# Performance work log

Measured on AMD Instinct MI355X. Metric: run time of the kernel, lower is better.

## Reference

```python
import jax, jax.numpy as jnp
import numpy as np
from jax import lax

N_FFT = 1024
HOP = 256
FFT_BIN = N_FFT // 2 + 1  # 513


def make_stft_kernel(n_fft: int) -> jnp.ndarray:
    """Fixed DFT basis kernel, shape (2*fft_bin, 1, n_fft), windowed with periodic Hann."""
    fft_bin = n_fft // 2 + 1
    # torch.linspace(0, 1, n_fft) is endpoint-inclusive, same as jnp.linspace
    t = jnp.linspace(0.0, 1.0, n_fft, dtype=jnp.float32)[None, None, :]
    k = jnp.arange(fft_bin, dtype=jnp.float32)[:, None, None]
    xt = t * k * (2.0 * jnp.pi)
    kernel = jnp.concatenate([jnp.cos(xt), jnp.sin(xt)], axis=0)  # (2*fft_bin, 1, n_fft)
    # torch.hann_window is periodic: 0.5*(1 - cos(2*pi*n/N))
    n = jnp.arange(n_fft, dtype=jnp.float32)
    hann = 0.5 * (1.0 - jnp.cos(2.0 * jnp.pi * n / n_fft))
    return kernel * hann[None, None, :]


def setup_inputs() -> dict:
    key = jax.random.key(0)
    x = jax.random.normal(key, (16, 1, 262144), dtype=jnp.float32)
    kernel = make_stft_kernel(N_FFT)
    return {"x": x, "kernel": kernel}


def reference(x, kernel):
    # padding == 'center'
    left = N_FFT // 2
    right = N_FFT - left
    x = jnp.pad(x, ((0, 0), (0, 0), (left, right)))
    # strided conv1d with fixed DFT-basis kernel
    y = lax.conv_general_dilated(
        x, kernel,
        window_strides=(HOP,),
        padding='VALID',
        dimension_numbers=('NCW', 'OIW', 'NCW'),
    )  # (B, 2*fft_bin, num_frames)
    real, imag = jnp.split(y, 2, axis=1)
    return real, imag
```

## Files before the change

kernel.cpp:

```cpp
#include <hip/hip_runtime.h>
#include <hip/hip_bf16.h>

#define NFFT    1024
#define HOPSZ   256
#define XLEN    262144
#define PADLEN  (XLEN + NFFT)
#define NBATCH  16
#define NBINS2  1026
#define FBIN    513
#define NFRAMES 1025
#define NGF     (NBATCH * NFRAMES)
#define TOTOUT  ((size_t)NBATCH * FBIN * NFRAMES)

#define KT 64
#define NKT 16
#define NWG 1024
#define BUFE 16384
#define BUFB 32768
#define LDS_BYTES (2 * BUFB)
#define NTAIL  49184
#define PSTRIDE 132

#define PX_BLKS 2056
#define PW_BLKS 1026

typedef short bf16x8 __attribute__((ext_vector_type(8)));
typedef float f32x4  __attribute__((ext_vector_type(4)));
typedef unsigned short u16x8 __attribute__((ext_vector_type(8)));
typedef unsigned short u16x4 __attribute__((ext_vector_type(4)));

__device__ __forceinline__ unsigned short f2bf(float f) {
  union { float f; unsigned u; } v; v.f = f;
  unsigned r = v.u + 0x7fffu + ((v.u >> 16) & 1u);
  return (unsigned short)(r >> 16);
}
__device__ __forceinline__ float bf2f(unsigned short h) {
  union { unsigned u; float f; } v; v.u = ((unsigned)h) << 16; return v.f;
}

typedef __attribute__((address_space(1))) void void_g;
typedef __attribute__((address_space(3))) void void_l;
__device__ __forceinline__ void gload_lds16(const void* g, void* l) {
  __builtin_amdgcn_global_load_lds((void_g*)(g), (void_l*)(l), 16, 0, 0);
}

__global__ __launch_bounds__(256) void pack_kernel(const float* __restrict__ x,
                                                   const float* __restrict__ W,
                                                   unsigned short* __restrict__ xp,
                                                   unsigned short* __restrict__ wb) {
  const int bid = blockIdx.x;
  const int tid = threadIdx.x;
  if (bid < PX_BLKS) {
    long long base = ((long long)bid * 256 + tid) * 8;
    int b   = (int)(base / PADLEN);
    int pos = (int)(base % PADLEN);
    const float* xb = x + (long long)b * XLEN;
    u16x8 v;
#pragma unroll
    for (int j = 0; j < 8; ++j) {
      int xi = pos + j - (NFFT / 2);
      float f = ((unsigned)xi < (unsigned)XLEN) ? xb[xi] : 0.0f;
      v[j] = f2bf(f);
    }
    *reinterpret_cast<u16x8*>(xp + base) = v;
  } else {
    long long t = (((long long)(bid - PX_BLKS)) * 256 + tid) * 4;
    float4 f = *reinterpret_cast<const float4*>(W + t);
    u16x4 v;
    v[0] = f2bf(f.x); v[1] = f2bf(f.y); v[2] = f2bf(f.z); v[3] = f2bf(f.w);
    *reinterpret_cast<u16x4*>(wb + t) = v;
  }
}

__global__ __launch_bounds__(256, 2) void stft_mfma128_kernel(const unsigned short* __restrict__ Xp,
                                                              const unsigned short* __restrict__ Wb,
                                                              float* __restrict__ out) {
  extern __shared__ unsigned short lds[];
  const int tid = threadIdx.x;
  const int l   = tid & 63;
  const int w   = tid >> 6;
  const int wr  = w >> 1;
  const int wc  = w & 1;
  const int r16 = l & 15, hi = l >> 4;

  const int bid   = blockIdx.x;
  const int xcd   = bid & 7;
  const int local = bid >> 3;
  const int nt    = xcd * 16 + (local >> 3);
  const int mt    = local & 7;
  const int bin0  = mt * 128;
  const int gf0   = nt * 128;

  const int lr = l >> 3;
  const int ls = l & 7;
  const int cswz = ((ls ^ lr) << 3);

  unsigned aqoff[4], boff[4];
#pragma unroll
  for (int q = 0; q < 4; ++q)
    aqoff[q] = (unsigned)(bin0 + (w * 4 + q) * 8 + lr) * NFFT + cswz;
#pragma unroll
  for (int j = 0; j < 4; ++j) {
    const int gf = gf0 + (w * 4 + j) * 8 + lr;
    const int bb = gf / NFRAMES;
    const int fr = gf - bb * NFRAMES;
    boff[j] = (unsigned)bb * PADLEN + (unsigned)fr * HOPSZ + cswz;
  }

#define STAGE(D, KC) do { \
    _Pragma("unroll") \
    for (int q_ = 0; q_ < 4; ++q_) \
      gload_lds16(Wb + aqoff[q_] + (KC), lds + (D) * BUFE + (w * 4 + q_) * 512); \
    _Pragma("unroll") \
    for (int j_ = 0; j_ < 4; ++j_) \
      gload_lds16(Xp + boff[j_] + (KC), lds + (D) * BUFE + 8192 + (w * 4 + j_) * 512); \
    } while (0)

  const int aB0 = (wr * 64 + r16) * 128;
  const int bB0 = 16384 + (wc * 64 + r16) * 128;
  const int swz = (r16 & 7) << 4;
  const int c0  = (hi * 16) ^ swz;
  const int c1  = (64 + hi * 16) ^ swz;

#define RD8(BASE, C, AARR, BARR) do { \
    _Pragma("unroll") \
    for (int n_ = 0; n_ < 4; ++n_) \
      BARR[n_] = *reinterpret_cast<const bf16x8*>((const char*)(BASE) + bB0 + n_ * 2048 + (C)); \
    _Pragma("unroll") \
    for (int m_ = 0; m_ < 4; ++m_) \
      AARR[m_] = *reinterpret_cast<const bf16x8*>((const char*)(BASE) + aB0 + m_ * 2048 + (C)); \
    } while (0)

#define MFMA16(AARR, BARR) do { \
    __builtin_amdgcn_s_setprio(1); \
    _Pragma("unroll") \
    for (int m_ = 0; m_ < 4; ++m_) { \
      _Pragma("unroll") \
      for (int n_ = 0; n_ < 4; ++n_) \
        acc[m_][n_] = __builtin_amdgcn_mfma_f32_16x16x32_bf16(AARR[m_], BARR[n_], acc[m_][n_], 0, 0, 0); \
    } \
    __builtin_amdgcn_s_setprio(0); } while (0)

  f32x4 acc[4][4] = {};
  bf16x8 A0[4], B0[4], A1[4], B1[4];

  STAGE(0, 0);
  STAGE(1, KT);
  asm volatile("s_waitcnt vmcnt(8)" ::: "memory");
  __builtin_amdgcn_s_barrier();
  __builtin_amdgcn_sched_barrier(0);
  RD8(lds, c0, A0, B0);

#pragma unroll 1
  for (int t = 0; t < NKT; ++t) {
    const int ci = t & 1;
    const char* cbuf = (const char*)lds + ci * BUFB;
    const char* nbuf = (const char*)lds + (ci ^ 1) * BUFB;
    const int kc2 = (t + 2) << 6;

    RD8(cbuf, c1, A1, B1);
    __builtin_amdgcn_sched_barrier(0);
    asm volatile("s_waitcnt lgkmcnt(8)" ::: "memory");
    __builtin_amdgcn_sched_barrier(0);
    MFMA16(A0, B0);

    asm volatile("s_waitcnt vmcnt(0) lgkmcnt(0)" ::: "memory");
    __builtin_amdgcn_sched_barrier(0);
    __builtin_amdgcn_s_barrier();
    __builtin_amdgcn_sched_barrier(0);
    if (t < NKT - 1) RD8(nbuf, c0, A0, B0);
    if (t < NKT - 2) STAGE(ci, kc2);
    __builtin_amdgcn_sched_barrier(0);
    MFMA16(A1, B1);
  }

  {
    float* patch = (float*)lds;
    const int col   = l & 15;
    const int rbase = (l >> 4) * 4;
    const int colbase = wc * 64;

    size_t baseR[2];
#pragma unroll
    for (int j = 0; j < 2; ++j) {
      const int gf = gf0 + j * 64 + l;
      const int bb = gf / NFRAMES;
      const int fr = gf - bb * NFRAMES;
      baseR[j] = (size_t)bb * FBIN * NFRAMES + fr;
    }

#pragma unroll
    for (int c = 0; c < 2; ++c) {
      __builtin_amdgcn_s_barrier();
      if (wr == c) {
#pragma unroll
        for (int m = 0; m < 4; ++m)
#pragma unroll
          for (int n = 0; n < 4; ++n)
#pragma unroll
            for (int r = 0; r < 4; ++r)
              patch[(m * 16 + rbase + r) * PSTRIDE + colbase + n * 16 + col] = acc[m][n][r];
      }
      __builtin_amdgcn_s_barrier();

      for (int i = 0; i < 16; ++i) {
        const int row = i * 4 + w;
        const int bin = bin0 + c * 64 + row;
        const size_t binoff = (size_t)bin * NFRAMES;
#pragma unroll
        for (int j = 0; j < 2; ++j) {
          const float v = patch[row * PSTRIDE + j * 64 + l];
          size_t off = binoff + (bin < FBIN ? baseR[j]
                                            : baseR[j] + TOTOUT - (size_t)FBIN * NFRAMES);
          out[off] = v;
        }
      }
    }
  }
#undef STAGE
#undef RD8
#undef MFMA16
}

__global__ __launch_bounds__(512) void stft_tail_kernel(const unsigned short* __restrict__ Xp,
                                                        const unsigned short* __restrict__ Wb,
                                                        float* __restrict__ out) {
  const int wid = (int)((blockIdx.x * 512 + threadIdx.x) >> 6);
  const int l   = threadIdx.x & 63;
  if (wid >= NTAIL) return;
  int bin, gf;
  if (wid < 2 * NGF) { bin = 1024 + (wid & 1); gf = wid >> 1; }
  else { const int s = wid - 2 * NGF; gf = 16384 + (s & 15); bin = s >> 4; }
  const int bb = gf / NFRAMES;
  const int fr = gf - bb * NFRAMES;
  const unsigned short* xr = Xp + (size_t)bb * PADLEN + (size_t)fr * HOPSZ + l * 16;
  const unsigned short* wr = Wb + (size_t)bin * NFFT + l * 16;
  u16x8 x0 = *reinterpret_cast<const u16x8*>(xr);
  u16x8 x1 = *reinterpret_cast<const u16x8*>(xr + 8);
  u16x8 w0 = *reinterpret_cast<const u16x8*>(wr);
  u16x8 w1 = *reinterpret_cast<const u16x8*>(wr + 8);
  float s0 = 0.f, s1 = 0.f;
#pragma unroll
  for (int j = 0; j < 8; ++j) {
    s0 = fmaf(bf2f(x0[j]), bf2f(w0[j]), s0);
    s1 = fmaf(bf2f(x1[j]), bf2f(w1[j]), s1);
  }
  float s = s0 + s1;
#pragma unroll
  for (int k = 32; k >= 1; k >>= 1) s += __shfl_xor(s, k);
  if (l == 0) {
    size_t off;
    if (bin < FBIN) off = ((size_t)bb * FBIN + bin) * NFRAMES + fr;
    else            off = TOTOUT + ((size_t)bb * FBIN + (bin - FBIN)) * NFRAMES + fr;
    out[off] = s;
  }
}

__global__ void stft_direct_kernel(const float* __restrict__ x, const float* __restrict__ W,
                                   float* __restrict__ out,
                                   int bin_lo, int nbins, int fr_lo, int nframes) {
  long long total = (long long)NBATCH * nbins * nframes;
  for (long long t = (long long)blockIdx.x * blockDim.x + threadIdx.x; t < total;
       t += (long long)gridDim.x * blockDim.x) {
    int fr = fr_lo + (int)(t % nframes);
    long long q = t / nframes;
    int bin = bin_lo + (int)(q % nbins);
    int b   = (int)(q / nbins);
    const float* xb = x + (long long)b * XLEN;
    const float* wrow = W + (long long)bin * NFFT;
    float s = 0.f;
    const int base = fr * HOPSZ - (NFFT / 2);
    for (int j = 0; j < NFFT; ++j) {
      int xi = base + j;
      float xv = ((unsigned)xi < (unsigned)XLEN) ? xb[xi] : 0.f;
      s = fmaf(xv, wrow[j], s);
    }
    size_t off;
    if (bin < FBIN) off = ((size_t)b * FBIN + bin) * NFRAMES + fr;
    else            off = TOTOUT + ((size_t)b * FBIN + (bin - FBIN)) * NFRAMES + fr;
    out[off] = s;
  }
}

extern "C" void kernel_launch(void* const* d_in, const int* in_sizes, int n_in,
                              void* d_out, int out_size, void* d_ws, size_t ws_size,
                              hipStream_t stream) {
  const float* x = (const float*)d_in[0];
  const float* W = (const float*)d_in[1];
  float* out = (float*)d_out;

  const size_t xp_bytes = (size_t)NBATCH * PADLEN * sizeof(unsigned short);
  const size_t wb_bytes = (size_t)NBINS2 * NFFT * sizeof(unsigned short);

  if (ws_size >= xp_bytes + wb_bytes) {
    unsigned short* xp = (unsigned short*)d_ws;
    unsigned short* wb = (unsigned short*)((char*)d_ws + xp_bytes);

    pack_kernel<<<PX_BLKS + PW_BLKS, 256, 0, stream>>>(x, W, xp, wb);
    stft_mfma128_kernel<<<NWG, 256, LDS_BYTES, stream>>>(xp, wb, out);
    stft_tail_kernel<<<NTAIL / 8, 512, 0, stream>>>(xp, wb, out);
  } else {
    stft_direct_kernel<<<2048, 256, 0, stream>>>(x, W, out, 0, NBINS2, 0, NFRAMES);
  }
}
```

Before: 66.09 us.

## Give each wave private LDS staging buffers to drop workgroup barriers

The shared double-buffered LDS tiles are replaced by per-wave private buffers. Each wave now stages only the A rows and B frames it consumes, with K-step 32 over 32 steps. The workgroup s_barrier in the main loop is removed, and synchronisation relies only on per-wave vmcnt/lgkmcnt waits. This gives up cross-wave sharing of staged tiles, so global/L2 traffic rises (each A and B row is loaded by two waves), and a new XOR swizzle is used for the smaller 64-byte rows.

```diff
diff --git a/kernel.cpp b/kernel.cpp
--- a/kernel.cpp
+++ b/kernel.cpp
@@ -12,12 +12,10 @@
 #define NGF     (NBATCH * NFRAMES)
 #define TOTOUT  ((size_t)NBATCH * FBIN * NFRAMES)
 
-#define KT 64
-#define NKT 16
+#define KT 32
+#define NKT 32
 #define NWG 1024
-#define BUFE 16384
-#define BUFB 32768
-#define LDS_BYTES (2 * BUFB)
+#define LDS_BYTES 65536
 #define NTAIL  49184
 #define PSTRIDE 132
 
@@ -91,44 +89,44 @@
   const int bin0  = mt * 128;
   const int gf0   = nt * 128;
 
-  const int lr = l >> 3;
-  const int ls = l & 7;
-  const int cswz = ((ls ^ lr) << 3);
+  const int lr = l >> 2;
+  const int ls = l & 3;
+  const int cswz = ((ls ^ ((lr >> 2) & 3)) << 3);
+  const int arow0 = bin0 + wr * 64;
+  const int brow0 = gf0 + wc * 64;
 
   unsigned aqoff[4], boff[4];
 #pragma unroll
   for (int q = 0; q < 4; ++q)
-    aqoff[q] = (unsigned)(bin0 + (w * 4 + q) * 8 + lr) * NFFT + cswz;
-#pragma unroll
-  for (int j = 0; j < 4; ++j) {
-    const int gf = gf0 + (w * 4 + j) * 8 + lr;
+    aqoff[q] = (unsigned)(arow0 + q * 16 + lr) * NFFT + cswz;
+#pragma unroll
+  for (int q = 0; q < 4; ++q) {
+    const int gf = brow0 + q * 16 + lr;
     const int bb = gf / NFRAMES;
     const int fr = gf - bb * NFRAMES;
-    boff[j] = (unsigned)bb * PADLEN + (unsigned)fr * HOPSZ + cswz;
-  }
+    boff[q] = (unsigned)bb * PADLEN + (unsigned)fr * HOPSZ + cswz;
+  }
+
+  unsigned short* wlds = lds + w * 8192;
 
 #define STAGE(D, KC) do { \
     _Pragma("unroll") \
     for (int q_ = 0; q_ < 4; ++q_) \
-      gload_lds16(Wb + aqoff[q_] + (KC), lds + (D) * BUFE + (w * 4 + q_) * 512); \
-    _Pragma("unroll") \
-    for (int j_ = 0; j_ < 4; ++j_) \
-      gload_lds16(Xp + boff[j_] + (KC), lds + (D) * BUFE + 8192 + (w * 4 + j_) * 512); \
+      gload_lds16(Wb + aqoff[q_] + (KC), (D) + q_ * 512); \
+    _Pragma("unroll") \
+    for (int q_ = 0; q_ < 4; ++q_) \
+      gload_lds16(Xp + boff[q_] + (KC), (D) + 2048 + q_ * 512); \
     } while (0)
 
-  const int aB0 = (wr * 64 + r16) * 128;
-  const int bB0 = 16384 + (wc * 64 + r16) * 128;
-  const int swz = (r16 & 7) << 4;
-  const int c0  = (hi * 16) ^ swz;
-  const int c1  = (64 + hi * 16) ^ swz;
-
-#define RD8(BASE, C, AARR, BARR) do { \
+  const int rdoff = r16 * 64 + ((hi ^ ((r16 >> 2) & 3)) << 4);
+
+#define RD8(BASE, AARR, BARR) do { \
     _Pragma("unroll") \
     for (int n_ = 0; n_ < 4; ++n_) \
-      BARR[n_] = *reinterpret_cast<const bf16x8*>((const char*)(BASE) + bB0 + n_ * 2048 + (C)); \
+      BARR[n_] = *reinterpret_cast<const bf16x8*>((BASE) + 4096 + n_ * 1024 + rdoff); \
     _Pragma("unroll") \
     for (int m_ = 0; m_ < 4; ++m_) \
-      AARR[m_] = *reinterpret_cast<const bf16x8*>((const char*)(BASE) + aB0 + m_ * 2048 + (C)); \
+      AARR[m_] = *reinterpret_cast<const bf16x8*>((BASE) + m_ * 1024 + rdoff); \
     } while (0)
 
 #define MFMA16(AARR, BARR) do { \
@@ -141,38 +139,45 @@
     } \
     __builtin_amdgcn_s_setprio(0); } while (0)
 
+#define LGKM0  asm volatile("s_waitcnt lgkmcnt(0)" ::: "memory"); __builtin_amdgcn_sched_barrier(0)
+#define VM8    asm volatile("s_waitcnt vmcnt(8)" ::: "memory");  __builtin_amdgcn_sched_barrier(0)
+#define SCHED0 __builtin_amdgcn_sched_barrier(0)
+
   f32x4 acc[4][4] = {};
   bf16x8 A0[4], B0[4], A1[4], B1[4];
 
-  STAGE(0, 0);
-  STAGE(1, KT);
-  asm volatile("s_waitcnt vmcnt(8)" ::: "memory");
-  __builtin_amdgcn_s_barrier();
-  __builtin_amdgcn_sched_barrier(0);
-  RD8(lds, c0, A0, B0);
+  const char* cb0 = (const char*)wlds;
+  const char* cb1 = (const char*)wlds + 8192;
+
+  STAGE(wlds, 0);
+  STAGE(wlds + 4096, KT);
+  VM8;
+  RD8(cb0, A0, B0);
 
 #pragma unroll 1
-  for (int t = 0; t < NKT; ++t) {
-    const int ci = t & 1;
-    const char* cbuf = (const char*)lds + ci * BUFB;
-    const char* nbuf = (const char*)lds + (ci ^ 1) * BUFB;
-    const int kc2 = (t + 2) << 6;
-
-    RD8(cbuf, c1, A1, B1);
-    __builtin_amdgcn_sched_barrier(0);
-    asm volatile("s_waitcnt lgkmcnt(8)" ::: "memory");
-    __builtin_amdgcn_sched_barrier(0);
+  for (int tt = 0; tt < 15; ++tt) {
+    const int t0 = tt * 2;
+    LGKM0;
+    STAGE(wlds, (t0 + 2) << 5);
+    VM8;
+    RD8(cb1, A1, B1);
+    SCHED0;
     MFMA16(A0, B0);
-
-    asm volatile("s_waitcnt vmcnt(0) lgkmcnt(0)" ::: "memory");
-    __builtin_amdgcn_sched_barrier(0);
-    __builtin_amdgcn_s_barrier();
-    __builtin_amdgcn_sched_barrier(0);
-    if (t < NKT - 1) RD8(nbuf, c0, A0, B0);
-    if (t < NKT - 2) STAGE(ci, kc2);
-    __builtin_amdgcn_sched_barrier(0);
+    LGKM0;
+    STAGE(wlds + 4096, (t0 + 3) << 5);
+    VM8;
+    RD8(cb0, A0, B0);
+    SCHED0;
     MFMA16(A1, B1);
   }
+  LGKM0;
+  asm volatile("s_waitcnt vmcnt(0)" ::: "memory");
+  SCHED0;
+  RD8(cb1, A1, B1);
+  SCHED0;
+  MFMA16(A0, B0);
+  LGKM0;
+  MFMA16(A1, B1);
 
   {
     float* patch = (float*)lds;
@@ -220,6 +225,9 @@
 #undef STAGE
 #undef RD8
 #undef MFMA16
+#undef LGKM0
+#undef VM8
+#undef SCHED0
 }
 
 __global__ __launch_bounds__(512) void stft_tail_kernel(const unsigned short* __restrict__ Xp,
```

Result: slower. 84.52 us (+27.9%).
